# Performance work log

Measured on AMD Instinct MI355X. Metric: run time of the kernel, lower is better.

Reference implementation:

```python
import jax, jax.numpy as jnp
import numpy as np

MAX_RADIUS = 0.2
MIN_RADIUS = 0.0
SAMPLE_NUM = 32
CHANNEL = 64
EPS = 1e-5


def _ball_query(points, centers):
    """points (B,N,3), centers (B,M,3) -> idx (B,M,S) int32.
    Mimics pointnet2 ball_query: first SAMPLE_NUM point indices within
    [MIN_RADIUS, MAX_RADIUS); slots past the last found repeat the first
    found index (0 if the ball is empty)."""
    d2 = jnp.sum((centers[:, :, None, :] - points[:, None, :, :]) ** 2, axis=-1)  # (B,M,N)
    mask = (d2 < MAX_RADIUS ** 2) & (d2 >= MIN_RADIUS ** 2)
    N = points.shape[1]
    scores = jnp.where(mask, jnp.arange(N, dtype=jnp.int32), jnp.int32(N))
    neg_vals, _ = jax.lax.top_k(-scores, SAMPLE_NUM)  # k smallest indices
    idx = -neg_vals  # (B,M,S), invalid slots == N
    first = idx[..., :1]
    first = jnp.where(first == N, 0, first)
    idx = jnp.where(idx == N, first, idx)
    return idx


def setup_inputs() -> dict:
    key = jax.random.key(0)
    k1, k2, k3, k4 = jax.random.split(key, 4)
    B, N, M, C = 4, 16384, 2048, CHANNEL
    return {
        "points_xyz": jax.random.uniform(k1, (B, N, 3), dtype=jnp.float32),
        "center_xyz": jax.random.uniform(k2, (B, M, 3), dtype=jnp.float32),
        "center_feature": jax.random.normal(k3, (B, M, C), dtype=jnp.float32),
        "features": jax.random.normal(k4, (B, C, N), dtype=jnp.float32),
        "affine_alpha": jnp.ones((1, 1, 1, C + 3), dtype=jnp.float32),
        "affine_beta": jnp.zeros((1, 1, 1, C + 3), dtype=jnp.float32),
    }


def reference(points_xyz, center_xyz, center_feature, features, affine_alpha, affine_beta):
    idx = _ball_query(points_xyz, center_xyz)  # (B,M,S)
    gather = jax.vmap(lambda a, i: a[i])  # per-batch fancy gather
    grouped_xyz = gather(points_xyz, idx)                      # (B,M,S,3)
    grouped_feat = gather(jnp.swapaxes(features, 1, 2), idx)   # (B,M,S,C)
    nf = jnp.concatenate([grouped_xyz, grouped_feat], axis=-1)  # (B,M,S,3+C)
    mean = jnp.concatenate([center_xyz, center_feature], axis=-1)[:, :, None, :]
    centered = nf - mean
    B = nf.shape[0]
    # torch.std default: unbiased (ddof=1), one scalar per batch element
    std = jnp.std(centered.reshape(B, -1), axis=-1, ddof=1).reshape(B, 1, 1, 1)
    out = affine_alpha * (centered / (std + EPS)) + affine_beta  # (B,M,S,3+C)
    return jnp.transpose(out, (0, 3, 1, 2))  # (B,3+C,M,S)
```

## Files before the change

kernel.cpp:

```cpp
#include <hip/hip_runtime.h>
#include <cstdint>
#include <cstddef>

#define B_ 4
#define N_ 16384
#define M_ 2048
#define C_ 64
#define S_ 32
#define J_ 67
#define R2_ 0.04f
#define EPS_ 1e-5f

__global__ __launch_bounds__(256) void k_phase1(
        const float* __restrict__ feat, float* __restrict__ featT,
        const float* __restrict__ pts, const float* __restrict__ ctr,
        int* __restrict__ idx_ws) {
    __shared__ float tile[64][65];
    int blk = blockIdx.x;
    int tid = threadIdx.x;

    if (blk < 1024) {
        int b  = blk >> 8;
        int n0 = (blk & 255) << 6;
        int r = tid >> 6, i = tid & 63;
        const float* fb = feat + (size_t)b * C_ * N_;
        #pragma unroll
        for (int cc = r; cc < 64; cc += 4)
            tile[cc][i] = fb[(size_t)cc * N_ + n0 + i];
        __syncthreads();
        float* ftb = featT + (size_t)b * N_ * C_;
        #pragma unroll
        for (int nn = r; nn < 64; nn += 4)
            ftb[(size_t)(n0 + nn) * C_ + i] = tile[i][nn];
        return;
    }

    int* sidx = (int*)&tile[0][0];
    int w    = tid >> 6;
    int lane = tid & 63;
    int bm   = (blk - 1024) * 4 + w;
    int b    = bm >> 11;
    const float* pb = pts + (size_t)b * N_ * 3;
    float cx = ctr[(size_t)bm * 3 + 0];
    float cy = ctr[(size_t)bm * 3 + 1];
    float cz = ctr[(size_t)bm * 3 + 2];

    float xs[4], ys[4], zs[4], xn[4], yn[4], zn[4];
    #pragma unroll
    for (int r = 0; r < 4; r++) {
        int i = r * 64 + lane;
        xs[r] = pb[i * 3 + 0]; ys[r] = pb[i * 3 + 1]; zs[r] = pb[i * 3 + 2];
    }
    int cnt = 0;
    for (int base = 0; base < N_; base += 256) {
        int nxt = base + 256;
        if (nxt < N_) {
            #pragma unroll
            for (int r = 0; r < 4; r++) {
                int i = nxt + r * 64 + lane;
                xn[r] = pb[i * 3 + 0]; yn[r] = pb[i * 3 + 1]; zn[r] = pb[i * 3 + 2];
            }
        }
        #pragma unroll
        for (int r = 0; r < 4; r++) {
            float dx = __fsub_rn(cx, xs[r]);
            float dy = __fsub_rn(cy, ys[r]);
            float dz = __fsub_rn(cz, zs[r]);
            float d2 = __fadd_rn(__fadd_rn(__fmul_rn(dx, dx), __fmul_rn(dy, dy)),
                                 __fmul_rn(dz, dz));
            bool in = d2 < R2_;
            unsigned long long mk = __ballot(in);
            int rank = __popcll(mk & ((1ull << lane) - 1ull));
            int pos = cnt + rank;
            if (in && pos < S_) sidx[w * S_ + pos] = base + r * 64 + lane;
            cnt += __popcll(mk);
            if (cnt >= S_) break;
        }
        if (cnt >= S_ || nxt >= N_) break;
        #pragma unroll
        for (int r = 0; r < 4; r++) { xs[r] = xn[r]; ys[r] = yn[r]; zs[r] = zn[r]; }
    }
    __syncthreads();
    int cfound = cnt < S_ ? cnt : S_;
    if (lane < S_) {
        int first = (cfound > 0) ? sidx[w * S_] : 0;
        int v = (lane < cfound) ? sidx[w * S_ + lane] : first;
        idx_ws[(size_t)bm * S_ + lane] = v;
    }
}

__global__ __launch_bounds__(256) void k_sums(
        const float* __restrict__ pts, const float* __restrict__ ctr,
        const float* __restrict__ featT, const float* __restrict__ cfeat,
        const int* __restrict__ idx_ws, float* __restrict__ partials) {
    int w    = threadIdx.x >> 6;
    int lane = threadIdx.x & 63;
    #pragma unroll
    for (int cc = 0; cc < 2; cc++) {
        int bm = blockIdx.x * 8 + w * 2 + cc;
        int b  = bm >> 11;
        const float* pb  = pts + (size_t)b * N_ * 3;
        const float* ftb = featT + (size_t)b * N_ * C_;
        int id = idx_ws[(size_t)bm * S_ + (lane & 31)];
        float cf = cfeat[(size_t)bm * C_ + lane];
        float cx = ctr[(size_t)bm * 3 + 0];
        float cy = ctr[(size_t)bm * 3 + 1];
        float cz = ctr[(size_t)bm * 3 + 2];

        float s1 = 0.f, s2 = 0.f;
        float v[S_];
        #pragma unroll
        for (int s = 0; s < S_; s++) {
            int p = __shfl(id, s);
            v[s] = ftb[(size_t)p * C_ + lane];
        }
        #pragma unroll
        for (int s = 0; s < S_; s++) {
            float d = v[s] - cf;
            s1 += d; s2 += d * d;
        }
        float cj = (lane < 32) ? cx : cy;
        float pv = pb[id * 3 + (lane >> 5)];
        float d = pv - cj; s1 += d; s2 += d * d;
        if (lane < 32) {
            float dz = pb[id * 3 + 2] - cz;
            s1 += dz; s2 += dz * dz;
        }
        #pragma unroll
        for (int off = 32; off > 0; off >>= 1) {
            s1 += __shfl_down(s1, off);
            s2 += __shfl_down(s2, off);
        }
        if (lane == 0) {
            partials[(size_t)bm * 2 + 0] = s1;
            partials[(size_t)bm * 2 + 1] = s2;
        }
    }
}

__global__ __launch_bounds__(256) void k_reduce(const float* __restrict__ partials,
                                                float* __restrict__ accum) {
    int b = blockIdx.x, tid = threadIdx.x;
    float s1 = 0.f, s2 = 0.f;
    for (int i = tid; i < M_; i += 256) {
        s1 += partials[((size_t)b * M_ + i) * 2 + 0];
        s2 += partials[((size_t)b * M_ + i) * 2 + 1];
    }
    __shared__ float l1[256], l2[256];
    l1[tid] = s1; l2[tid] = s2;
    __syncthreads();
    for (int off = 128; off > 0; off >>= 1) {
        if (tid < off) { l1[tid] += l1[tid + off]; l2[tid] += l2[tid + off]; }
        __syncthreads();
    }
    if (tid == 0) {
        float sum = l1[0], sumsq = l2[0];
        const float n = (float)(M_ * S_ * J_);
        float mean = sum / n;
        float var  = (sumsq - sum * mean) / (n - 1.f);
        accum[b] = 1.f / (sqrtf(var) + EPS_);
    }
}

__global__ __launch_bounds__(256) void k_output(
        const float* __restrict__ pts, const float* __restrict__ ctr,
        const float* __restrict__ featT, const float* __restrict__ cfeat,
        const float* __restrict__ alpha, const float* __restrict__ beta,
        const int* __restrict__ idx_ws, const float* __restrict__ accum,
        float* __restrict__ out) {
    int blk = blockIdx.x;
    int b  = blk >> 8;
    int mt = blk & 255;
    int tid = threadIdx.x;
    int mi = tid >> 5;
    int s  = tid & 31;
    int m  = mt * 8 + mi;
    size_t bm = (size_t)b * M_ + m;
    int p = idx_ws[bm * S_ + s];
    float inv = accum[b];

    const float* pb = pts + (size_t)b * N_ * 3;
    size_t obase = ((size_t)b * J_ * M_ + m) * S_ + s;
    #pragma unroll
    for (int j = 0; j < 3; j++) {
        float v = pb[p * 3 + j] - ctr[bm * 3 + j];
        out[obase + (size_t)j * M_ * S_] = alpha[j] * inv * v + beta[j];
    }
    const float4* fr4 = (const float4*)(featT + ((size_t)b * N_ + p) * C_);
    const float4* cf4 = (const float4*)(cfeat + bm * C_);
    #pragma unroll
    for (int cq = 0; cq < 16; cq++) {
        float4 fv = fr4[cq];
        float4 cv = cf4[cq];
        int j = 3 + cq * 4;
        out[obase + (size_t)(j + 0) * M_ * S_] = alpha[j + 0] * inv * (fv.x - cv.x) + beta[j + 0];
        out[obase + (size_t)(j + 1) * M_ * S_] = alpha[j + 1] * inv * (fv.y - cv.y) + beta[j + 1];
        out[obase + (size_t)(j + 2) * M_ * S_] = alpha[j + 2] * inv * (fv.z - cv.z) + beta[j + 2];
        out[obase + (size_t)(j + 3) * M_ * S_] = alpha[j + 3] * inv * (fv.w - cv.w) + beta[j + 3];
    }
}

extern "C" void kernel_launch(void* const* d_in, const int* in_sizes, int n_in,
                              void* d_out, int out_size, void* d_ws, size_t ws_size,
                              hipStream_t stream) {
    const float* pts   = (const float*)d_in[0];
    const float* ctr   = (const float*)d_in[1];
    const float* cfeat = (const float*)d_in[2];
    const float* feat  = (const float*)d_in[3];
    const float* alpha = (const float*)d_in[4];
    const float* beta  = (const float*)d_in[5];
    float* out = (float*)d_out;

    char* ws = (char*)d_ws;
    float* featT    = (float*)ws;
    int*   idx_ws   = (int*)(ws + (size_t)B_ * N_ * C_ * 4);
    float* partials = (float*)(ws + (size_t)B_ * N_ * C_ * 4 + (size_t)B_ * M_ * S_ * 4);
    float* accum    = partials + (size_t)B_ * M_ * 2;

    k_phase1<<<3072, 256, 0, stream>>>(feat, featT, pts, ctr, idx_ws);
    k_sums<<<B_ * M_ / 8, 256, 0, stream>>>(pts, ctr, featT, cfeat, idx_ws, partials);
    k_reduce<<<B_, 256, 0, stream>>>(partials, accum);
    k_output<<<B_ * (M_ / 8), 256, 0, stream>>>(pts, ctr, featT, cfeat, alpha, beta,
                                                idx_ws, accum, out);
}
```

Baseline: 51.57 us.

## Fold std reduction into sums/output kernels, vectorize output stores, deepen ball-query prefetch

Removes the separate k_reduce launch. k_sums now reduces each block's 8 centers in shared memory and writes per-block partials, and every k_output block re-reduces its batch's 256 partials before writing. k_output is restructured so each thread handles 4 samples and issues float4 stores along S, and it runs on fewer blocks. The ball-query loop double-buffers two 256-point chunks to keep more loads in flight. The costs are redundant reduction work per output block, fewer output blocks, and more registers in phase 1.

```diff
diff --git a/kernel.cpp b/kernel.cpp
--- a/kernel.cpp
+++ b/kernel.cpp
@@ -10,6 +10,28 @@
 #define J_ 67
 #define R2_ 0.04f
 #define EPS_ 1e-5f
+
+
+#define LD3(X, Y, Z, BASE)                                             \
+    for (int r = 0; r < 4; r++) {                                      \
+        int i = (BASE) + r * 64 + lane;                                \
+        X[r] = pb[i * 3 + 0]; Y[r] = pb[i * 3 + 1]; Z[r] = pb[i * 3 + 2]; \
+    }
+
+#define PROC3(X, Y, Z, BASE)                                           \
+    for (int r = 0; r < 4; r++) {                                      \
+        float dx = __fsub_rn(cx, X[r]);                                \
+        float dy = __fsub_rn(cy, Y[r]);                                \
+        float dz = __fsub_rn(cz, Z[r]);                                \
+        float d2 = __fadd_rn(__fadd_rn(__fmul_rn(dx, dx), __fmul_rn(dy, dy)), \
+                             __fmul_rn(dz, dz));                       \
+        bool in = d2 < R2_;                                            \
+        unsigned long long mk = __ballot(in);                          \
+        int rank = __popcll(mk & ((1ull << lane) - 1ull));             \
+        int pos = cnt + rank;                                          \
+        if (in && pos < S_) sidx[w * S_ + pos] = (BASE) + r * 64 + lane; \
+        cnt += __popcll(mk);                                           \
+    }
 
 __global__ __launch_bounds__(256) void k_phase1(
         const float* __restrict__ feat, float* __restrict__ featT,
@@ -45,40 +67,25 @@
     float cy = ctr[(size_t)bm * 3 + 1];
     float cz = ctr[(size_t)bm * 3 + 2];
 
-    float xs[4], ys[4], zs[4], xn[4], yn[4], zn[4];
-    #pragma unroll
-    for (int r = 0; r < 4; r++) {
-        int i = r * 64 + lane;
-        xs[r] = pb[i * 3 + 0]; ys[r] = pb[i * 3 + 1]; zs[r] = pb[i * 3 + 2];
-    }
+    float ax[4], ay[4], az[4], bx[4], by[4], bz[4];
+    float px[4], py[4], pz[4], qx[4], qy[4], qz[4];
     int cnt = 0;
-    for (int base = 0; base < N_; base += 256) {
-        int nxt = base + 256;
-        if (nxt < N_) {
-            #pragma unroll
-            for (int r = 0; r < 4; r++) {
-                int i = nxt + r * 64 + lane;
-                xn[r] = pb[i * 3 + 0]; yn[r] = pb[i * 3 + 1]; zn[r] = pb[i * 3 + 2];
-            }
-        }
-        #pragma unroll
+    LD3(ax, ay, az, 0)
+    LD3(bx, by, bz, 256)
+    for (int base = 0; base < N_; base += 512) {
+        int nb = base + 512;
+        if (nb < N_) {
+            LD3(px, py, pz, nb)
+            LD3(qx, qy, qz, nb + 256)
+        }
+        PROC3(ax, ay, az, base)
+        if (cnt >= S_) break;
+        PROC3(bx, by, bz, base + 256)
+        if (cnt >= S_ || nb >= N_) break;
         for (int r = 0; r < 4; r++) {
-            float dx = __fsub_rn(cx, xs[r]);
-            float dy = __fsub_rn(cy, ys[r]);
-            float dz = __fsub_rn(cz, zs[r]);
-            float d2 = __fadd_rn(__fadd_rn(__fmul_rn(dx, dx), __fmul_rn(dy, dy)),
-                                 __fmul_rn(dz, dz));
-            bool in = d2 < R2_;
-            unsigned long long mk = __ballot(in);
-            int rank = __popcll(mk & ((1ull << lane) - 1ull));
-            int pos = cnt + rank;
-            if (in && pos < S_) sidx[w * S_ + pos] = base + r * 64 + lane;
-            cnt += __popcll(mk);
-            if (cnt >= S_) break;
-        }
-        if (cnt >= S_ || nxt >= N_) break;
-        #pragma unroll
-        for (int r = 0; r < 4; r++) { xs[r] = xn[r]; ys[r] = yn[r]; zs[r] = zn[r]; }
+            ax[r] = px[r]; ay[r] = py[r]; az[r] = pz[r];
+            bx[r] = qx[r]; by[r] = qy[r]; bz[r] = qz[r];
+        }
     }
     __syncthreads();
     int cfound = cnt < S_ ? cnt : S_;
@@ -92,12 +99,14 @@
 __global__ __launch_bounds__(256) void k_sums(
         const float* __restrict__ pts, const float* __restrict__ ctr,
         const float* __restrict__ featT, const float* __restrict__ cfeat,
-        const int* __restrict__ idx_ws, float* __restrict__ partials) {
+        const int* __restrict__ idx_ws, float* __restrict__ bpart) {
+    __shared__ float pp1[8], pp2[8];
     int w    = threadIdx.x >> 6;
     int lane = threadIdx.x & 63;
     #pragma unroll
     for (int cc = 0; cc < 2; cc++) {
-        int bm = blockIdx.x * 8 + w * 2 + cc;
+        int ci = w * 2 + cc;
+        int bm = blockIdx.x * 8 + ci;
         int b  = bm >> 11;
         const float* pb  = pts + (size_t)b * N_ * 3;
         const float* ftb = featT + (size_t)b * N_ * C_;
@@ -115,50 +124,25 @@
             v[s] = ftb[(size_t)p * C_ + lane];
         }
         #pragma unroll
-        for (int s = 0; s < S_; s++) {
-            float d = v[s] - cf;
-            s1 += d; s2 += d * d;
-        }
+        for (int s = 0; s < S_; s++) { float d = v[s] - cf; s1 += d; s2 += d * d; }
         float cj = (lane < 32) ? cx : cy;
         float pv = pb[id * 3 + (lane >> 5)];
-        float d = pv - cj; s1 += d; s2 += d * d;
-        if (lane < 32) {
-            float dz = pb[id * 3 + 2] - cz;
-            s1 += dz; s2 += dz * dz;
-        }
+        float d0 = pv - cj; s1 += d0; s2 += d0 * d0;
+        if (lane < 32) { float dz = pb[id * 3 + 2] - cz; s1 += dz; s2 += dz * dz; }
         #pragma unroll
         for (int off = 32; off > 0; off >>= 1) {
             s1 += __shfl_down(s1, off);
             s2 += __shfl_down(s2, off);
         }
-        if (lane == 0) {
-            partials[(size_t)bm * 2 + 0] = s1;
-            partials[(size_t)bm * 2 + 1] = s2;
-        }
-    }
-}
-
-__global__ __launch_bounds__(256) void k_reduce(const float* __restrict__ partials,
-                                                float* __restrict__ accum) {
-    int b = blockIdx.x, tid = threadIdx.x;
-    float s1 = 0.f, s2 = 0.f;
-    for (int i = tid; i < M_; i += 256) {
-        s1 += partials[((size_t)b * M_ + i) * 2 + 0];
-        s2 += partials[((size_t)b * M_ + i) * 2 + 1];
-    }
-    __shared__ float l1[256], l2[256];
-    l1[tid] = s1; l2[tid] = s2;
+        if (lane == 0) { pp1[ci] = s1; pp2[ci] = s2; }
+    }
     __syncthreads();
-    for (int off = 128; off > 0; off >>= 1) {
-        if (tid < off) { l1[tid] += l1[tid + off]; l2[tid] += l2[tid + off]; }
-        __syncthreads();
-    }
-    if (tid == 0) {
-        float sum = l1[0], sumsq = l2[0];
-        const float n = (float)(M_ * S_ * J_);
-        float mean = sum / n;
-        float var  = (sumsq - sum * mean) / (n - 1.f);
-        accum[b] = 1.f / (sqrtf(var) + EPS_);
+    if (threadIdx.x == 0) {
+        float a1 = 0.f, a2 = 0.f;
+        #pragma unroll
+        for (int i = 0; i < 8; i++) { a1 += pp1[i]; a2 += pp2[i]; }
+        bpart[blockIdx.x * 2 + 0] = a1;
+        bpart[blockIdx.x * 2 + 1] = a2;
     }
 }
 
@@ -166,37 +150,71 @@
         const float* __restrict__ pts, const float* __restrict__ ctr,
         const float* __restrict__ featT, const float* __restrict__ cfeat,
         const float* __restrict__ alpha, const float* __restrict__ beta,
-        const int* __restrict__ idx_ws, const float* __restrict__ accum,
+        const int* __restrict__ idx_ws, const float* __restrict__ bpart,
         float* __restrict__ out) {
-    int blk = blockIdx.x;
-    int b  = blk >> 8;
-    int mt = blk & 255;
-    int tid = threadIdx.x;
-    int mi = tid >> 5;
-    int s  = tid & 31;
-    int m  = mt * 8 + mi;
-    size_t bm = (size_t)b * M_ + m;
-    int p = idx_ws[bm * S_ + s];
-    float inv = accum[b];
-
-    const float* pb = pts + (size_t)b * N_ * 3;
-    size_t obase = ((size_t)b * J_ * M_ + m) * S_ + s;
+    __shared__ float r1[256], r2[256];
+    int blk = blockIdx.x, tid = threadIdx.x;
+    int batch = blk >> 6;
+
+    const float* bp = bpart + (size_t)batch * 256 * 2;
+    r1[tid] = bp[tid * 2 + 0];
+    r2[tid] = bp[tid * 2 + 1];
+    __syncthreads();
+    for (int off = 128; off > 0; off >>= 1) {
+        if (tid < off) { r1[tid] += r1[tid + off]; r2[tid] += r2[tid + off]; }
+        __syncthreads();
+    }
+    float sum = r1[0], sumsq = r2[0];
+    const float n = (float)(M_ * S_ * J_);
+    float mean = sum / n;
+    float var  = (sumsq - sum * mean) / (n - 1.f);
+    float inv  = 1.f / (sqrtf(var) + EPS_);
+
+    int m  = (blk & 63) * 32 + (tid >> 3);
+    int sq = tid & 7;
+    int s0 = sq * 4;
+    size_t bm = (size_t)batch * M_ + m;
+    int4 pidx = *(const int4*)(idx_ws + bm * S_ + s0);
+    const float* pb = pts + (size_t)batch * N_ * 3;
+    size_t obase = ((size_t)batch * J_ * M_ + m) * (size_t)S_ + s0;
+
     #pragma unroll
     for (int j = 0; j < 3; j++) {
-        float v = pb[p * 3 + j] - ctr[bm * 3 + j];
-        out[obase + (size_t)j * M_ * S_] = alpha[j] * inv * v + beta[j];
-    }
-    const float4* fr4 = (const float4*)(featT + ((size_t)b * N_ + p) * C_);
-    const float4* cf4 = (const float4*)(cfeat + bm * C_);
-    #pragma unroll
+        float a = alpha[j] * inv, bt = beta[j];
+        float cj = ctr[bm * 3 + j];
+        float4 o;
+        o.x = a * (pb[pidx.x * 3 + j] - cj) + bt;
+        o.y = a * (pb[pidx.y * 3 + j] - cj) + bt;
+        o.z = a * (pb[pidx.z * 3 + j] - cj) + bt;
+        o.w = a * (pb[pidx.w * 3 + j] - cj) + bt;
+        *(float4*)(out + obase + (size_t)j * (M_ * S_)) = o;
+    }
+    const float4* f0 = (const float4*)(featT + ((size_t)batch * N_ + pidx.x) * C_);
+    const float4* f1 = (const float4*)(featT + ((size_t)batch * N_ + pidx.y) * C_);
+    const float4* f2 = (const float4*)(featT + ((size_t)batch * N_ + pidx.z) * C_);
+    const float4* f3 = (const float4*)(featT + ((size_t)batch * N_ + pidx.w) * C_);
+    const float4* cf = (const float4*)(cfeat + bm * C_);
+    #pragma unroll 2
     for (int cq = 0; cq < 16; cq++) {
-        float4 fv = fr4[cq];
-        float4 cv = cf4[cq];
+        float4 v0 = f0[cq], v1 = f1[cq], v2 = f2[cq], v3 = f3[cq], c = cf[cq];
         int j = 3 + cq * 4;
-        out[obase + (size_t)(j + 0) * M_ * S_] = alpha[j + 0] * inv * (fv.x - cv.x) + beta[j + 0];
-        out[obase + (size_t)(j + 1) * M_ * S_] = alpha[j + 1] * inv * (fv.y - cv.y) + beta[j + 1];
-        out[obase + (size_t)(j + 2) * M_ * S_] = alpha[j + 2] * inv * (fv.z - cv.z) + beta[j + 2];
-        out[obase + (size_t)(j + 3) * M_ * S_] = alpha[j + 3] * inv * (fv.w - cv.w) + beta[j + 3];
+        float a0 = alpha[j + 0] * inv, b0 = beta[j + 0];
+        float a1 = alpha[j + 1] * inv, b1 = beta[j + 1];
+        float a2 = alpha[j + 2] * inv, b2 = beta[j + 2];
+        float a3 = alpha[j + 3] * inv, b3 = beta[j + 3];
+        float4 o0, o1, o2, o3;
+        o0.x = a0 * (v0.x - c.x) + b0; o0.y = a0 * (v1.x - c.x) + b0;
+        o0.z = a0 * (v2.x - c.x) + b0; o0.w = a0 * (v3.x - c.x) + b0;
+        o1.x = a1 * (v0.y - c.y) + b1; o1.y = a1 * (v1.y - c.y) + b1;
+        o1.z = a1 * (v2.y - c.y) + b1; o1.w = a1 * (v3.y - c.y) + b1;
+        o2.x = a2 * (v0.z - c.z) + b2; o2.y = a2 * (v1.z - c.z) + b2;
+        o2.z = a2 * (v2.z - c.z) + b2; o2.w = a2 * (v3.z - c.z) + b2;
+        o3.x = a3 * (v0.w - c.w) + b3; o3.y = a3 * (v1.w - c.w) + b3;
+        o3.z = a3 * (v2.w - c.w) + b3; o3.w = a3 * (v3.w - c.w) + b3;
+        *(float4*)(out + obase + (size_t)(j + 0) * (M_ * S_)) = o0;
+        *(float4*)(out + obase + (size_t)(j + 1) * (M_ * S_)) = o1;
+        *(float4*)(out + obase + (size_t)(j + 2) * (M_ * S_)) = o2;
+        *(float4*)(out + obase + (size_t)(j + 3) * (M_ * S_)) = o3;
     }
 }
 
@@ -212,14 +230,12 @@
     float* out = (float*)d_out;
 
     char* ws = (char*)d_ws;
-    float* featT    = (float*)ws;
-    int*   idx_ws   = (int*)(ws + (size_t)B_ * N_ * C_ * 4);
-    float* partials = (float*)(ws + (size_t)B_ * N_ * C_ * 4 + (size_t)B_ * M_ * S_ * 4);
-    float* accum    = partials + (size_t)B_ * M_ * 2;
+    float* featT = (float*)ws;
+    int*   idx_ws = (int*)(ws + (size_t)B_ * N_ * C_ * 4);
+    float* bpart = (float*)(ws + (size_t)B_ * N_ * C_ * 4 + (size_t)B_ * M_ * S_ * 4);
 
     k_phase1<<<3072, 256, 0, stream>>>(feat, featT, pts, ctr, idx_ws);
-    k_sums<<<B_ * M_ / 8, 256, 0, stream>>>(pts, ctr, featT, cfeat, idx_ws, partials);
-    k_reduce<<<B_, 256, 0, stream>>>(partials, accum);
-    k_output<<<B_ * (M_ / 8), 256, 0, stream>>>(pts, ctr, featT, cfeat, alpha, beta,
-                                                idx_ws, accum, out);
-}
+    k_sums<<<B_ * M_ / 8, 256, 0, stream>>>(pts, ctr, featT, cfeat, idx_ws, bpart);
+    k_output<<<256, 256, 0, stream>>>(pts, ctr, featT, cfeat, alpha, beta,
+                                      idx_ws, bpart, out);
+}
```

New measurement: 65.41 us. 26.8% more time.
